# Kernel optimization log

Hardware: AMD Instinct MI355X
Metric: run time of the kernel (lower is better)

Reference implementation:

```python
import jax, jax.numpy as jnp
import numpy as np

MARGIN = 0.1
PERM_SEED = 42  # fixed stand-in for torch.randperm per row


def setup_inputs() -> dict:
    key = jax.random.key(0)
    k1, k2, k3 = jax.random.split(key, 3)
    n, d, f = 32768, 1000, 300
    inputs = jax.random.normal(k1, (n, f), dtype=jnp.float32)
    Y = jax.random.normal(k2, (d, f), dtype=jnp.float32)
    y_idxs = jax.random.randint(k3, (n,), 0, d)
    return {"inputs": inputs, "Y": Y, "y_idxs": y_idxs}


def reference(inputs, Y, y_idxs):
    # inputs: [n, f], Y: [d, f] class semantic embeddings, y_idxs: [n]
    n, d = inputs.shape[0], Y.shape[0]

    # All dot products at once: S[i, j] = Y[j] . inputs[i]
    S = inputs @ Y.T  # [n, d]

    # One random class permutation per row (torch.randperm(d) per sample)
    perm_keys = jax.random.split(jax.random.key(PERM_SEED), n)
    perms = jax.vmap(lambda k: jax.random.permutation(k, d))(perm_keys)  # [n, d]

    ap = S[jnp.arange(n), y_idxs]                 # [n]   anchor-positive dots
    an = jnp.take_along_axis(S, perms, axis=1)    # [n, d] anchor-negative dots in perm order

    valid = perms != y_idxs[:, None]              # skip j == y
    # early-break condition at each permutation slot
    cond = valid & ((ap[:, None] - an) > MARGIN)
    c = cond.astype(jnp.int32)
    excl_cum = jnp.cumsum(c, axis=1) - c          # exclusive cumsum of break events
    # include every valid slot up to AND including the first breaking slot
    include = valid & (excl_cum == 0)             # [n, d]

    # MarginRankingLoss with target=1: mean(max(0, margin + an - ap))
    per_pair = jnp.maximum(0.0, MARGIN + an - ap[:, None])
    total = jnp.sum(jnp.where(include, per_pair, 0.0))
    count = jnp.maximum(jnp.sum(include), 1).astype(jnp.float32)
    return total / count
```

## Files before the change

kernel.cpp:

```cpp
#include <hip/hip_runtime.h>
#include <stdint.h>

#define N_ROWS 32768
#define D_CLS  1000
#define D_PAD  1024
#define F_DIM  300
#define F_PAD  320
#define MARGIN 0.1f

#define BM     128
#define BN     128
#define BK     64
#define GTHR   512
#define KGTHR  1024
#define LDTA   328
#define LDTB   72

#define M_PB   32
#define NTHR   512
#define NT_PW  8
#define MT_PB  2
#define LDA    328
#define SROW   34

#define NPART  32

typedef short short8 __attribute__((ext_vector_type(8)));
typedef float f32x4  __attribute__((ext_vector_type(4)));

__device__ __forceinline__ uint32_t rotl32(uint32_t x, int r) {
  return (x << r) | (x >> (32 - r));
}

__device__ __forceinline__ void threefry2x32(uint32_t k0, uint32_t k1,
                                             uint32_t x0, uint32_t x1,
                                             uint32_t& o0, uint32_t& o1) {
  uint32_t k2 = k0 ^ k1 ^ 0x1BD11BDAu;
  x0 += k0; x1 += k1;
#define TF_R(r) { x0 += x1; x1 = rotl32(x1, (r)); x1 ^= x0; }
  TF_R(13) TF_R(15) TF_R(26) TF_R(6)
  x0 += k1; x1 += k2 + 1u;
  TF_R(17) TF_R(29) TF_R(16) TF_R(24)
  x0 += k2; x1 += k0 + 2u;
  TF_R(13) TF_R(15) TF_R(26) TF_R(6)
  x0 += k0; x1 += k1 + 3u;
  TF_R(17) TF_R(29) TF_R(16) TF_R(24)
  x0 += k1; x1 += k2 + 4u;
  TF_R(13) TF_R(15) TF_R(26) TF_R(6)
  x0 += k2; x1 += k0 + 5u;
#undef TF_R
  o0 = x0; o1 = x1;
}

struct TFSched {
  uint32_t k0, k1, k2, k2p1, k0p2, k1p3, k2p4, k0p5;
};
__device__ __forceinline__ TFSched tf_make(uint32_t k0, uint32_t k1) {
  TFSched s;
  s.k0 = k0; s.k1 = k1;
  s.k2 = k0 ^ k1 ^ 0x1BD11BDAu;
  s.k2p1 = s.k2 + 1u; s.k0p2 = k0 + 2u; s.k1p3 = k1 + 3u;
  s.k2p4 = s.k2 + 4u; s.k0p5 = k0 + 5u;
  return s;
}
__device__ __forceinline__ uint32_t tf_hash(const TFSched& s, uint32_t c) {
  uint32_t x0 = s.k0, x1 = c + s.k1;
#define TFH(r) { x0 += x1; x1 = __builtin_amdgcn_alignbit(x1, x1, 32 - (r)); x1 ^= x0; }
  TFH(13) TFH(15) TFH(26) TFH(6)
  x0 += s.k1; x1 += s.k2p1;
  TFH(17) TFH(29) TFH(16) TFH(24)
  x0 += s.k2; x1 += s.k0p2;
  TFH(13) TFH(15) TFH(26) TFH(6)
  x0 += s.k0; x1 += s.k1p3;
  TFH(17) TFH(29) TFH(16) TFH(24)
  x0 += s.k1; x1 += s.k2p4;
  TFH(13) TFH(15) TFH(26) TFH(6)
  x0 += s.k2; x1 += s.k0p5;
#undef TFH
  return x0 ^ x1;
}

__device__ __forceinline__ uint16_t f2bf(float f) {
  uint32_t u = __builtin_bit_cast(uint32_t, f);
  return (uint16_t)((u + 0x7FFFu + ((u >> 16) & 1u)) >> 16);
}
__device__ __forceinline__ float bf2f(uint16_t v) {
  return __builtin_bit_cast(float, (uint32_t)v << 16);
}
__device__ __forceinline__ float bf2f_lo(uint32_t v) {
  return __builtin_bit_cast(float, v << 16);
}
__device__ __forceinline__ float bf2f_hi(uint32_t v) {
  return __builtin_bit_cast(float, v & 0xFFFF0000u);
}

__device__ __forceinline__ void keygen_rp(uint32_t* __restrict__ keyP,
                                          const uint32_t* __restrict__ subk,
                                          int r0, int rp_loc, int lane) {
  const size_t rpg = (size_t)(r0 >> 1) + rp_loc;
  const int rA = r0 + 2 * rp_loc;
  const uint4 sk4 = *(const uint4*)(subk + 2 * rA);
  const TFSched sA = tf_make(sk4.x, sk4.y);
  const TFSched sB = tf_make(sk4.z, sk4.w);
#pragma unroll
  for (int chunk = 0; chunk < 4; ++chunk) {
    const uint32_t c0 = (uint32_t)(chunk * 256 + 4 * lane);
    uint32_t o[4];
#pragma unroll
    for (int j = 0; j < 4; ++j) {
      uint32_t kA = tf_hash(sA, c0 + (uint32_t)j);
      uint32_t kB = tf_hash(sB, c0 + (uint32_t)j);
      o[j] = (kA >> 16) | (kB & 0xFFFF0000u);
    }
    uint4 ov; ov.x = o[0]; ov.y = o[1]; ov.z = o[2]; ov.w = o[3];
    *(uint4*)(keyP + (rpg << 10) + c0) = ov;
  }
}

__global__ void prep(const float* __restrict__ Y, uint16_t* __restrict__ Ybf,
                     uint32_t* __restrict__ subk) {
  int i = blockIdx.x * 256 + threadIdx.x;
  if (i < D_PAD * F_PAD) {
    int j = i / F_PAD;
    int k = i - j * F_PAD;
    float v = (j < D_CLS && k < F_DIM) ? Y[j * F_DIM + k] : 0.f;
    Ybf[i] = f2bf(v);
  }
  if (i < N_ROWS) {
    uint32_t r1, r2, s1, s2;
    threefry2x32(0u, 42u, 0u, (uint32_t)i, r1, r2);
    threefry2x32(r1, r2, 0u, 1u, s1, s2);
    subk[2 * i]     = s1;
    subk[2 * i + 1] = s2;
  }
}

__launch_bounds__(KGTHR, 4)
__global__ void gk2(const float* __restrict__ inputs,
                    const uint16_t* __restrict__ Ybf,
                    uint32_t* __restrict__ Spair,
                    uint32_t* __restrict__ keyP,
                    const uint32_t* __restrict__ subk) {
  __shared__ __align__(16) uint16_t A_lds[BM * LDTA];

  const int t    = threadIdx.x;
  const int wave = t >> 6;
  const int lane = t & 63;
  const int l15  = lane & 15;
  const int g    = lane >> 4;
  const int r0   = blockIdx.x * BM;

  for (int i = t; i < BM * (F_DIM / 4); i += KGTHR) {
    int r  = i / 75;
    int c4 = i - r * 75;
    float4 v = *(const float4*)(inputs + (size_t)(r0 + r) * F_DIM + c4 * 4);
    ushort4 o;
    o.x = f2bf(v.x); o.y = f2bf(v.y); o.z = f2bf(v.z); o.w = f2bf(v.w);
    *(ushort4*)&A_lds[r * LDTA + c4 * 4] = o;
  }
  for (int i = t; i < BM * 7; i += KGTHR) {
    int r = i / 7, p = i - r * 7;
    *(ushort4*)&A_lds[r * LDTA + 300 + p * 4] = (ushort4){0, 0, 0, 0};
  }
  __syncthreads();

  if (wave < 8) {
    const int wm = wave >> 1;
    const int wn = wave & 1;
    const uint16_t* aBase = &A_lds[(wm * 32 + l15) * LDTA + g * 8];

#pragma unroll 1
    for (int cn = 0; cn < 8; ++cn) {
      f32x4 acc[2][4];
#pragma unroll
      for (int mt = 0; mt < 2; ++mt)
#pragma unroll
        for (int nt = 0; nt < 4; ++nt) acc[mt][nt] = (f32x4){0.f, 0.f, 0.f, 0.f};

      const uint16_t* gB[4];
#pragma unroll
      for (int nt = 0; nt < 4; ++nt) {
        const int col = cn * 128 + wn * 64 + nt * 16 + l15;
        gB[nt] = Ybf + (size_t)col * F_PAD + g * 8;
      }

#pragma unroll 2
      for (int ks = 0; ks < F_PAD / 32; ++ks) {
        short8 a[2], b[4];
#pragma unroll
        for (int nt = 0; nt < 4; ++nt)
          b[nt] = *(const short8*)(gB[nt] + ks * 32);
#pragma unroll
        for (int mt = 0; mt < 2; ++mt)
          a[mt] = *(const short8*)(aBase + mt * 16 * LDTA + ks * 32);
#pragma unroll
        for (int mt = 0; mt < 2; ++mt)
#pragma unroll
          for (int nt = 0; nt < 4; ++nt)
            acc[mt][nt] = __builtin_amdgcn_mfma_f32_16x16x32_bf16(a[mt], b[nt], acc[mt][nt], 0, 0, 0);
      }

#pragma unroll
      for (int mt = 0; mt < 2; ++mt)
#pragma unroll
        for (int nt = 0; nt < 4; ++nt) {
          const int col = cn * 128 + wn * 64 + nt * 16 + l15;
#pragma unroll
          for (int p = 0; p < 2; ++p) {
            uint32_t lo = f2bf(acc[mt][nt][2 * p]);
            uint32_t hi = f2bf(acc[mt][nt][2 * p + 1]);
            size_t rp = (size_t)(r0 >> 1) + wm * 16 + mt * 8 + g * 2 + p;
            Spair[rp * D_PAD + col] = (hi << 16) | lo;
          }
        }
    }
#pragma unroll 1
    for (int i = 0; i < 2; ++i)
      keygen_rp(keyP, subk, r0, 48 + wave * 2 + i, lane);
  } else {
    const int kw = wave - 8;
#pragma unroll 1
    for (int i = 0; i < 6; ++i)
      keygen_rp(keyP, subk, r0, kw * 6 + i, lane);
  }
}

__launch_bounds__(256, 4)
__global__ void loss_light(const uint32_t* __restrict__ Spair,
                           const uint32_t* __restrict__ keyP,
                           const int* __restrict__ yidx,
                           float* __restrict__ rowSum,
                           int* __restrict__ rowCnt) {
  const int lane = threadIdx.x & 63;
  const int wave = threadIdx.x >> 6;
  const int rp   = blockIdx.x * 4 + wave;
  const int rA   = 2 * rp;
  const int rB   = rA + 1;
  const int yA = yidx[rA], yB = yidx[rB];
  const uint32_t* Sp = Spair + (size_t)rp * D_PAD;
  const uint32_t* Kp = keyP  + (size_t)rp * D_PAD;
  const float apA = bf2f_lo(Sp[yA]);
  const float apB = bf2f_hi(Sp[yB]);

  uint32_t an[16], kk[16];
#pragma unroll
  for (int q4 = 0; q4 < 4; ++q4) {
    uint4 v = *(const uint4*)(Sp + q4 * 256 + lane * 4);
    an[4 * q4 + 0] = v.x; an[4 * q4 + 1] = v.y;
    an[4 * q4 + 2] = v.z; an[4 * q4 + 3] = v.w;
    uint4 w = *(const uint4*)(Kp + q4 * 256 + lane * 4);
    kk[4 * q4 + 0] = w.x; kk[4 * q4 + 1] = w.y;
    kk[4 * q4 + 2] = w.z; kk[4 * q4 + 3] = w.w;
  }

  uint32_t mnA = 0xFFFFu, mnB = 0xFFFFu;
#pragma unroll
  for (int q = 0; q < 16; ++q) {
    const int c = (q >> 2) * 256 + lane * 4 + (q & 3);
    const uint32_t kA = kk[q] & 0xFFFFu, kB = kk[q] >> 16;
    const float anA = bf2f_lo(an[q]), anB = bf2f_hi(an[q]);
    if ((c < D_CLS) && (c != yA) && (apA - anA) > MARGIN) mnA = (kA < mnA) ? kA : mnA;
    if ((c < D_CLS) && (c != yB) && (apB - anB) > MARGIN) mnB = (kB < mnB) ? kB : mnB;
  }
#pragma unroll
  for (int off = 1; off < 64; off <<= 1) {
    uint32_t oA = __shfl_xor(mnA, off, 64);
    uint32_t oB = __shfl_xor(mnB, off, 64);
    mnA = (oA < mnA) ? oA : mnA;
    mnB = (oB < mnB) ? oB : mnB;
  }

  float smA = 0.f, smB = 0.f; int ctA = 0, ctB = 0;
#pragma unroll
  for (int q = 0; q < 16; ++q) {
    const int c = (q >> 2) * 256 + lane * 4 + (q & 3);
    const uint32_t kA = kk[q] & 0xFFFFu, kB = kk[q] >> 16;
    const float anA = bf2f_lo(an[q]), anB = bf2f_hi(an[q]);
    if ((c < D_CLS) && (c != yA) && kA < mnA) { smA += MARGIN + anA - apA; ctA += 1; }
    if ((c < D_CLS) && (c != yB) && kB < mnB) { smB += MARGIN + anB - apB; ctB += 1; }
  }
#pragma unroll
  for (int off = 1; off < 64; off <<= 1) {
    smA += __shfl_xor(smA, off, 64);
    smB += __shfl_xor(smB, off, 64);
    ctA += __shfl_xor(ctA, off, 64);
    ctB += __shfl_xor(ctB, off, 64);
  }
  if (lane == 0) {
    rowSum[rA] = smA;  rowCnt[rA] = ctA + (mnA != 0xFFFFu ? 1 : 0);
    rowSum[rB] = smB;  rowCnt[rB] = ctB + (mnB != 0xFFFFu ? 1 : 0);
  }
}

__launch_bounds__(GTHR, 1)
__global__ void gemm_s(const float* __restrict__ inputs,
                       const uint16_t* __restrict__ Ybf,
                       uint32_t* __restrict__ Spair) {
  __shared__ __align__(16) uint16_t A_lds[BM * LDTA];
  __shared__ __align__(16) uint16_t B_lds[2][BN * LDTB];

  const int t    = threadIdx.x;
  const int wave = t >> 6;
  const int lane = t & 63;
  const int l15  = lane & 15;
  const int g    = lane >> 4;
  const int wm   = wave >> 1;
  const int wn   = wave & 1;
  const int r0   = blockIdx.x * BM;

  for (int i = t; i < BM * (F_DIM / 4); i += GTHR) {
    int r  = i / 75;
    int c4 = i - r * 75;
    float4 v = *(const float4*)(inputs + (size_t)(r0 + r) * F_DIM + c4 * 4);
    ushort4 o;
    o.x = f2bf(v.x); o.y = f2bf(v.y); o.z = f2bf(v.z); o.w = f2bf(v.w);
    *(ushort4*)&A_lds[r * LDTA + c4 * 4] = o;
  }
  for (int i = t; i < BM * 7; i += GTHR) {
    int r = i / 7, p = i - r * 7;
    *(ushort4*)&A_lds[r * LDTA + 300 + p * 4] = (ushort4){0, 0, 0, 0};
  }

  const int brow = t >> 3, bkof = t & 7;
  short8 bv[2];
  auto LOADB = [&](int tile) {
    const int c0 = (tile / 5) * BN;
    const int k0 = (tile % 5) * BK;
#pragma unroll
    for (int j = 0; j < 2; ++j)
      bv[j] = *(const short8*)(Ybf + (size_t)(c0 + j * 64 + brow) * F_PAD + k0 + bkof * 8);
  };
  auto WRITEB = [&](int buf) {
#pragma unroll
    for (int j = 0; j < 2; ++j)
      *(short8*)&B_lds[buf][(j * 64 + brow) * LDTB + bkof * 8] = bv[j];
  };

  f32x4 acc[2][4];
#pragma unroll
  for (int mt = 0; mt < 2; ++mt)
#pragma unroll
    for (int nt = 0; nt < 4; ++nt) acc[mt][nt] = (f32x4){0.f, 0.f, 0.f, 0.f};

  LOADB(0);
  __syncthreads();
  WRITEB(0);
  __syncthreads();

  const int NT = 8 * 5;
#pragma unroll 1
  for (int tile = 0; tile < NT; ++tile) {
    const int kt = tile % 5;
    if (tile < NT - 1) LOADB(tile + 1);
    const uint16_t* Bc = B_lds[tile & 1];
#pragma unroll
    for (int ks = 0; ks < 2; ++ks) {
      short8 a[2], b[4];
#pragma unroll
      for (int mt = 0; mt < 2; ++mt)
        a[mt] = *(const short8*)&A_lds[(wm * 32 + mt * 16 + l15) * LDTA + kt * BK + ks * 32 + g * 8];
#pragma unroll
      for (int nt = 0; nt < 4; ++nt)
        b[nt] = *(const short8*)&Bc[(wn * 64 + nt * 16 + l15) * LDTB + ks * 32 + g * 8];
#pragma unroll
      for (int mt = 0; mt < 2; ++mt)
#pragma unroll
        for (int nt = 0; nt < 4; ++nt)
          acc[mt][nt] = __builtin_amdgcn_mfma_f32_16x16x32_bf16(a[mt], b[nt], acc[mt][nt], 0, 0, 0);
    }
    if (kt == 4) {
      const int c0 = (tile / 5) * BN;
#pragma unroll
      for (int mt = 0; mt < 2; ++mt)
#pragma unroll
        for (int nt = 0; nt < 4; ++nt) {
          const int col = c0 + wn * 64 + nt * 16 + l15;
#pragma unroll
          for (int p = 0; p < 2; ++p) {
            uint32_t lo = f2bf(acc[mt][nt][2 * p]);
            uint32_t hi = f2bf(acc[mt][nt][2 * p + 1]);
            size_t rp = (size_t)(r0 >> 1) + wm * 16 + mt * 8 + g * 2 + p;
            Spair[rp * D_PAD + col] = (hi << 16) | lo;
          }
          acc[mt][nt] = (f32x4){0.f, 0.f, 0.f, 0.f};
        }
    }
    if (tile < NT - 1) {
      WRITEB((tile + 1) & 1);
      __syncthreads();
    }
  }
}

__launch_bounds__(256, 2)
__global__ void hash_loss(const uint32_t* __restrict__ Spair,
                          const uint32_t* __restrict__ subk,
                          const int* __restrict__ yidx,
                          float* __restrict__ rowSum,
                          int* __restrict__ rowCnt) {
  const int lane = threadIdx.x & 63;
  const int wave = threadIdx.x >> 6;
  const int rp   = blockIdx.x * 4 + wave;
  const int rA   = 2 * rp;
  const int rB   = 2 * rp + 1;

  const int yA = yidx[rA], yB = yidx[rB];
  const TFSched sA = tf_make(subk[2 * rA], subk[2 * rA + 1]);
  const TFSched sB = tf_make(subk[2 * rB], subk[2 * rB + 1]);

  const uint32_t* Sp = Spair + (size_t)rp * D_PAD;
  const float apA = bf2f_lo(Sp[yA]);
  const float apB = bf2f_hi(Sp[yB]);

  uint32_t an[16];
#pragma unroll
  for (int j = 0; j < 4; ++j) {
    uint4 v = *(const uint4*)(Sp + j * 256 + lane * 4);
    an[4 * j + 0] = v.x; an[4 * j + 1] = v.y;
    an[4 * j + 2] = v.z; an[4 * j + 3] = v.w;
  }

  uint32_t skAB[16];
  uint32_t pkA = 0xFFFFFFFFu, pkB = 0xFFFFFFFFu;
#pragma unroll
  for (int q = 0; q < 16; ++q) {
    const int c = (q >> 2) * 256 + lane * 4 + (q & 3);
    uint32_t kA = tf_hash(sA, (uint32_t)c);
    uint32_t kB = tf_hash(sB, (uint32_t)c);
    skAB[q] = (kA >> 16) | (kB & 0xFFFF0000u);
    float anA = bf2f_lo(an[q]);
    float anB = bf2f_hi(an[q]);
    if ((c < D_CLS) && (c != yA) && (apA - anA) > MARGIN) {
      pkA = (kA < pkA) ? kA : pkA;
    }
    if ((c < D_CLS) && (c != yB) && (apB - anB) > MARGIN) {
      pkB = (kB < pkB) ? kB : pkB;
    }
  }
#pragma unroll
  for (int off = 1; off < 64; off <<= 1) {
    uint32_t oA = __shfl_xor(pkA, off, 64);
    uint32_t oB = __shfl_xor(pkB, off, 64);
    pkA = (oA < pkA) ? oA : pkA;
    pkB = (oB < pkB) ? oB : pkB;
  }
  const uint32_t pA16 = pkA >> 16;
  const uint32_t pB16 = pkB >> 16;

  float smA = 0.f, smB = 0.f; int ctA = 0, ctB = 0;
#pragma unroll
  for (int q = 0; q < 16; ++q) {
    const int c = (q >> 2) * 256 + lane * 4 + (q & 3);
    float anA = bf2f_lo(an[q]);
    float anB = bf2f_hi(an[q]);
    if ((c < D_CLS) && (c != yA) && (skAB[q] & 0xFFFFu) < pA16) {
      smA += MARGIN + anA - apA; ctA += 1;
    }
    if ((c < D_CLS) && (c != yB) && (skAB[q] >> 16) < pB16) {
      smB += MARGIN + anB - apB; ctB += 1;
    }
  }
#pragma unroll
  for (int off = 1; off < 64; off <<= 1) {
    smA += __shfl_xor(smA, off, 64);
    smB += __shfl_xor(smB, off, 64);
    ctA += __shfl_xor(ctA, off, 64);
    ctB += __shfl_xor(ctB, off, 64);
  }
  if (lane == 0) {
    rowSum[rA] = smA;
    rowCnt[rA] = ctA + (pkA != 0xFFFFFFFFu ? 1 : 0);
    rowSum[rB] = smB;
    rowCnt[rB] = ctB + (pkB != 0xFFFFFFFFu ? 1 : 0);
  }
}

__launch_bounds__(NTHR, 4)
__global__ void triplet_fused(const float* __restrict__ inputs,
                              const uint16_t* __restrict__ Ybf,
                              const int* __restrict__ yidx,
                              float* __restrict__ rowSum,
                              int* __restrict__ rowCnt) {
  __shared__ __align__(16) uint16_t SH[D_PAD * SROW];
  __shared__ int      y_sh[M_PB];
  __shared__ uint32_t subk_sh[M_PB][2];

  const int t    = threadIdx.x;
  const int wave = t >> 6;
  const int lane = t & 63;
  const int l15  = lane & 15;
  const int g    = lane >> 4;
  const int row0 = blockIdx.x * M_PB;
  const int colbase = wave * (NT_PW * 16);

  if (t < M_PB) {
    y_sh[t] = yidx[row0 + t];
    uint32_t r1, r2, s1, s2;
    threefry2x32(0u, 42u, 0u, (uint32_t)(row0 + t), r1, r2);
    threefry2x32(r1, r2, 0u, 1u, s1, s2);
    subk_sh[t][0] = s1; subk_sh[t][1] = s2;
  }

  uint16_t* A_fl = SH;
  for (int i = t; i < M_PB * (F_DIM / 4); i += NTHR) {
    int r  = i / 75;
    int c4 = i - r * 75;
    float4 v = *(const float4*)(inputs + (size_t)(row0 + r) * F_DIM + c4 * 4);
    ushort4 o;
    o.x = f2bf(v.x); o.y = f2bf(v.y); o.z = f2bf(v.z); o.w = f2bf(v.w);
    *(ushort4*)&A_fl[r * LDA + c4 * 4] = o;
  }
  for (int i = t; i < M_PB * 5; i += NTHR) {
    int r = i / 5, p = i - r * 5;
    *(ushort4*)&A_fl[r * LDA + 300 + p * 4] = (ushort4){0, 0, 0, 0};
  }
  __syncthreads();

  f32x4 acc[MT_PB][NT_PW];
#pragma unroll
  for (int mt = 0; mt < MT_PB; ++mt)
#pragma unroll
    for (int nt = 0; nt < NT_PW; ++nt) acc[mt][nt] = (f32x4){0.f, 0.f, 0.f, 0.f};

  const uint16_t* gB[NT_PW];
#pragma unroll
  for (int nt = 0; nt < NT_PW; ++nt) {
    int j = colbase + nt * 16 + l15;
    gB[nt] = Ybf + (size_t)j * F_PAD + (g << 3);
  }
  const uint16_t* aBase = &A_fl[l15 * LDA + (g << 3)];

#pragma unroll 2
  for (int ks = 0; ks < F_PAD / 32; ++ks) {
    short8 b[NT_PW], a[MT_PB];
#pragma unroll
    for (int nt = 0; nt < NT_PW; ++nt)
      b[nt] = *(const short8*)(gB[nt] + ks * 32);
#pragma unroll
    for (int mt = 0; mt < MT_PB; ++mt)
      a[mt] = *(const short8*)(aBase + mt * 16 * LDA + ks * 32);
#pragma unroll
    for (int mt = 0; mt < MT_PB; ++mt)
#pragma unroll
      for (int nt = 0; nt < NT_PW; ++nt)
        acc[mt][nt] = __builtin_amdgcn_mfma_f32_16x16x32_bf16(a[mt], b[nt], acc[mt][nt], 0, 0, 0);
  }

  __syncthreads();

#pragma unroll
  for (int mt = 0; mt < MT_PB; ++mt)
#pragma unroll
    for (int nt = 0; nt < NT_PW; ++nt) {
      int col = colbase + nt * 16 + l15;
#pragma unroll
      for (int p = 0; p < 2; ++p) {
        uint32_t lo = f2bf(acc[mt][nt][2 * p]);
        uint32_t hi = f2bf(acc[mt][nt][2 * p + 1]);
        *(uint32_t*)&SH[col * SROW + mt * 16 + (g << 2) + 2 * p] = (hi << 16) | lo;
      }
    }
  __syncthreads();

#pragma unroll
  for (int pr = 0; pr < 2; ++pr) {
    const int rA = wave * 4 + pr * 2;
    const int rB = rA + 1;
    const int yA = y_sh[rA], yB = y_sh[rB];
    const uint32_t a1 = subk_sh[rA][0], a2 = subk_sh[rA][1];
    const uint32_t b1 = subk_sh[rB][0], b2 = subk_sh[rB][1];
    const float apA = bf2f(SH[yA * SROW + rA]);
    const float apB = bf2f(SH[yB * SROW + rB]);

    uint32_t skA[16], skB[16];
    uint32_t pkA = 0xFFFFFFFFu, pkB = 0xFFFFFFFFu;
#pragma unroll
    for (int q = 0; q < 16; ++q) {
      const int c = q * 64 + lane;
      uint32_t xA, yAo, xB, yBo;
      threefry2x32(a1, a2, 0u, (uint32_t)c, xA, yAo);
      threefry2x32(b1, b2, 0u, (uint32_t)c, xB, yBo);
      skA[q] = xA ^ yAo;
      skB[q] = xB ^ yBo;
      float anA = bf2f(SH[c * SROW + rA]);
      float anB = bf2f(SH[c * SROW + rB]);
      if ((c < D_CLS) && (c != yA) && (apA - anA) > MARGIN) {
        pkA = (skA[q] < pkA) ? skA[q] : pkA;
      }
      if ((c < D_CLS) && (c != yB) && (apB - anB) > MARGIN) {
        pkB = (skB[q] < pkB) ? skB[q] : pkB;
      }
    }
#pragma unroll
    for (int off = 1; off < 64; off <<= 1) {
      uint32_t oA = __shfl_xor(pkA, off, 64);
      uint32_t oB = __shfl_xor(pkB, off, 64);
      pkA = (oA < pkA) ? oA : pkA;
      pkB = (oB < pkB) ? oB : pkB;
    }
    float smA = 0.f, smB = 0.f; int ctA = 0, ctB = 0;
#pragma unroll
    for (int q = 0; q < 16; ++q) {
      const int c = q * 64 + lane;
      float anA = bf2f(SH[c * SROW + rA]);
      float anB = bf2f(SH[c * SROW + rB]);
      if ((c < D_CLS) && (c != yA) && skA[q] < pkA) { smA += MARGIN + anA - apA; ctA += 1; }
      if ((c < D_CLS) && (c != yB) && skB[q] < pkB) { smB += MARGIN + anB - apB; ctB += 1; }
    }
#pragma unroll
    for (int off = 1; off < 64; off <<= 1) {
      smA += __shfl_xor(smA, off, 64);
      smB += __shfl_xor(smB, off, 64);
      ctA += __shfl_xor(ctA, off, 64);
      ctB += __shfl_xor(ctB, off, 64);
    }
    if (lane == 0) {
      rowSum[row0 + rA] = smA;
      rowCnt[row0 + rA] = ctA + (pkA != 0xFFFFFFFFu ? 1 : 0);
      rowSum[row0 + rB] = smB;
      rowCnt[row0 + rB] = ctB + (pkB != 0xFFFFFFFFu ? 1 : 0);
    }
  }
}

__global__ void reduce_part(const float* __restrict__ rowSum,
                            const int* __restrict__ rowCnt,
                            float* __restrict__ pS, int* __restrict__ pC) {
  __shared__ float ss[4];
  __shared__ int   sc[4];
  const int base = blockIdx.x * (N_ROWS / NPART);
  float s = 0.f; int c = 0;
  for (int i = threadIdx.x; i < N_ROWS / NPART; i += 256) {
    s += rowSum[base + i];
    c += rowCnt[base + i];
  }
#pragma unroll
  for (int off = 32; off > 0; off >>= 1) {
    s += __shfl_down(s, (unsigned)off, 64);
    c += __shfl_down(c, (unsigned)off, 64);
  }
  int wid = threadIdx.x >> 6, lane = threadIdx.x & 63;
  if (lane == 0) { ss[wid] = s; sc[wid] = c; }
  __syncthreads();
  if (threadIdx.x == 0) {
    pS[blockIdx.x] = ss[0] + ss[1] + ss[2] + ss[3];
    pC[blockIdx.x] = sc[0] + sc[1] + sc[2] + sc[3];
  }
}

__global__ void reduce_final(const float* __restrict__ pS,
                             const int* __restrict__ pC,
                             float* __restrict__ out) {
  const int lane = threadIdx.x;
  float s = (lane < NPART) ? pS[lane] : 0.f;
  int   c = (lane < NPART) ? pC[lane] : 0;
#pragma unroll
  for (int off = 32; off > 0; off >>= 1) {
    s += __shfl_down(s, (unsigned)off, 64);
    c += __shfl_down(c, (unsigned)off, 64);
  }
  if (lane == 0) out[0] = s / (float)(c < 1 ? 1 : c);
}

extern "C" void kernel_launch(void* const* d_in, const int* in_sizes, int n_in,
                              void* d_out, int out_size, void* d_ws, size_t ws_size,
                              hipStream_t stream) {
  const float* inputs = (const float*)d_in[0];
  const float* Y      = (const float*)d_in[1];
  const int*   yidx   = (const int*)d_in[2];
  float* out = (float*)d_out;

  char* ws = (char*)d_ws;
  size_t off = 0;
  uint16_t* Ybf    = (uint16_t*)(ws + off); off += (size_t)D_PAD * F_PAD * 2;
  float*    rowSum = (float*)(ws + off);    off += (size_t)N_ROWS * 4;
  int*      rowCnt = (int*)(ws + off);      off += (size_t)N_ROWS * 4;
  uint32_t* subk   = (uint32_t*)(ws + off); off += (size_t)N_ROWS * 8;
  float*    pS     = (float*)(ws + off);    off += (size_t)NPART * 4;
  int*      pC     = (int*)(ws + off);      off += (size_t)NPART * 4;
  off = (off + 255) & ~(size_t)255;
  uint32_t* Spair  = (uint32_t*)(ws + off); off += (size_t)(N_ROWS / 2) * D_PAD * 4;
  const size_t need_mid = off;
  off = (off + 255) & ~(size_t)255;
  uint32_t* keyP   = (uint32_t*)(ws + off); off += (size_t)(N_ROWS / 2) * D_PAD * 4;
  const size_t need_full = off;

  hipLaunchKernelGGL(prep, dim3((D_PAD * F_PAD + 255) / 256), dim3(256),
                     0, stream, Y, Ybf, subk);
  if (ws_size >= need_full) {
    hipLaunchKernelGGL(gk2, dim3(N_ROWS / BM), dim3(KGTHR),
                       0, stream, inputs, Ybf, Spair, keyP, subk);
    hipLaunchKernelGGL(loss_light, dim3(N_ROWS / 8), dim3(256),
                       0, stream, Spair, keyP, yidx, rowSum, rowCnt);
  } else if (ws_size >= need_mid) {
    hipLaunchKernelGGL(gemm_s, dim3(N_ROWS / BM), dim3(GTHR),
                       0, stream, inputs, Ybf, Spair);
    hipLaunchKernelGGL(hash_loss, dim3(N_ROWS / 8), dim3(256),
                       0, stream, Spair, subk, yidx, rowSum, rowCnt);
  } else {
    hipLaunchKernelGGL(triplet_fused, dim3(N_ROWS / M_PB), dim3(NTHR),
                       0, stream, inputs, Ybf, yidx, rowSum, rowCnt);
  }
  hipLaunchKernelGGL(reduce_part, dim3(NPART), dim3(256), 0, stream,
                     rowSum, rowCnt, pS, pC);
  hipLaunchKernelGGL(reduce_final, dim3(1), dim3(64), 0, stream, pS, pC, out);
}
```

Measured before the change: 133.0 us.

## Split GEMM and permutation-key generation into separate interleaved blocks

Replaces the 1024-thread block, in which some waves ran the GEMM and others generated threefry permutation keys, with 512-thread blocks that each take one role. Role is chosen by a blockIdx bit, so GEMM and keygen blocks alternate in groups of eight. GEMM blocks now cover 64 rows with 8 waves each holding a 2x2 MFMA tile, and keygen blocks each handle 32 row pairs. The aim is better occupancy and overlap of compute-bound hashing with MFMA work across CUs. In exchange there are more blocks, each GEMM block loads B for fewer rows (more redundant Y reads), and LDS per block is smaller.

Result: slower. 187.9 us (+41.3%).

```diff
diff --git a/kernel.cpp b/kernel.cpp
--- a/kernel.cpp
+++ b/kernel.cpp
@@ -8,12 +8,17 @@
 #define F_PAD  320
 #define MARGIN 0.1f
 
+#define GBM    64
+#define GKTHR  512
+#define LDTA   328
+#define NGB    (N_ROWS / GBM)
+#define RP_PB  32
+#define NKB    ((N_ROWS / 2) / RP_PB)
+
 #define BM     128
 #define BN     128
 #define BK     64
 #define GTHR   512
-#define KGTHR  1024
-#define LDTA   328
 #define LDTB   72
 
 #define M_PB   32
@@ -94,11 +99,10 @@
   return __builtin_bit_cast(float, v & 0xFFFF0000u);
 }
 
-__device__ __forceinline__ void keygen_rp(uint32_t* __restrict__ keyP,
-                                          const uint32_t* __restrict__ subk,
-                                          int r0, int rp_loc, int lane) {
-  const size_t rpg = (size_t)(r0 >> 1) + rp_loc;
-  const int rA = r0 + 2 * rp_loc;
+__device__ __forceinline__ void keygen_rp_g(uint32_t* __restrict__ keyP,
+                                            const uint32_t* __restrict__ subk,
+                                            size_t rpg, int lane) {
+  const int rA = 2 * (int)rpg;
   const uint4 sk4 = *(const uint4*)(subk + 2 * rA);
   const TFSched sA = tf_make(sk4.x, sk4.y);
   const TFSched sB = tf_make(sk4.z, sk4.w);
@@ -135,76 +139,74 @@
   }
 }
 
-__launch_bounds__(KGTHR, 4)
-__global__ void gk2(const float* __restrict__ inputs,
+__launch_bounds__(GKTHR, 6)
+__global__ void gkb(const float* __restrict__ inputs,
                     const uint16_t* __restrict__ Ybf,
                     uint32_t* __restrict__ Spair,
                     uint32_t* __restrict__ keyP,
                     const uint32_t* __restrict__ subk) {
-  __shared__ __align__(16) uint16_t A_lds[BM * LDTA];
+  __shared__ __align__(16) uint16_t A_lds[GBM * LDTA];
 
   const int t    = threadIdx.x;
   const int wave = t >> 6;
   const int lane = t & 63;
   const int l15  = lane & 15;
   const int g    = lane >> 4;
-  const int r0   = blockIdx.x * BM;
-
-  for (int i = t; i < BM * (F_DIM / 4); i += KGTHR) {
-    int r  = i / 75;
-    int c4 = i - r * 75;
-    float4 v = *(const float4*)(inputs + (size_t)(r0 + r) * F_DIM + c4 * 4);
-    ushort4 o;
-    o.x = f2bf(v.x); o.y = f2bf(v.y); o.z = f2bf(v.z); o.w = f2bf(v.w);
-    *(ushort4*)&A_lds[r * LDTA + c4 * 4] = o;
-  }
-  for (int i = t; i < BM * 7; i += KGTHR) {
-    int r = i / 7, p = i - r * 7;
-    *(ushort4*)&A_lds[r * LDTA + 300 + p * 4] = (ushort4){0, 0, 0, 0};
-  }
-  __syncthreads();
-
-  if (wave < 8) {
-    const int wm = wave >> 1;
-    const int wn = wave & 1;
+  const int role = (blockIdx.x >> 3) & 1;
+  const int sub  = (blockIdx.x >> 4) * 8 + (blockIdx.x & 7);
+
+  if (role == 0) {
+    const int r0 = sub * GBM;
+
+    for (int i = t; i < GBM * (F_DIM / 4); i += GKTHR) {
+      int r  = i / 75;
+      int c4 = i - r * 75;
+      float4 v = *(const float4*)(inputs + (size_t)(r0 + r) * F_DIM + c4 * 4);
+      ushort4 o;
+      o.x = f2bf(v.x); o.y = f2bf(v.y); o.z = f2bf(v.z); o.w = f2bf(v.w);
+      *(ushort4*)&A_lds[r * LDTA + c4 * 4] = o;
+    }
+    for (int i = t; i < GBM * 7; i += GKTHR) {
+      int r = i / 7, p = i - r * 7;
+      *(ushort4*)&A_lds[r * LDTA + 300 + p * 4] = (ushort4){0, 0, 0, 0};
+    }
+    __syncthreads();
+
+    const int wm = wave >> 2;
+    const int wn = wave & 3;
     const uint16_t* aBase = &A_lds[(wm * 32 + l15) * LDTA + g * 8];
 
 #pragma unroll 1
     for (int cn = 0; cn < 8; ++cn) {
-      f32x4 acc[2][4];
+      f32x4 acc[2][2];
 #pragma unroll
       for (int mt = 0; mt < 2; ++mt)
 #pragma unroll
-        for (int nt = 0; nt < 4; ++nt) acc[mt][nt] = (f32x4){0.f, 0.f, 0.f, 0.f};
-
-      const uint16_t* gB[4];
-#pragma unroll
-      for (int nt = 0; nt < 4; ++nt) {
-        const int col = cn * 128 + wn * 64 + nt * 16 + l15;
-        gB[nt] = Ybf + (size_t)col * F_PAD + g * 8;
-      }
+        for (int nt = 0; nt < 2; ++nt) acc[mt][nt] = (f32x4){0.f, 0.f, 0.f, 0.f};
+
+      const uint16_t* gBp = Ybf + (size_t)(cn * 128 + wn * 32 + l15) * F_PAD + g * 8;
 
 #pragma unroll 2
       for (int ks = 0; ks < F_PAD / 32; ++ks) {
-        short8 a[2], b[4];
-#pragma unroll
-        for (int nt = 0; nt < 4; ++nt)
-          b[nt] = *(const short8*)(gB[nt] + ks * 32);
+        short8 a[2], b[2];
+#pragma unroll
+        for (int nt = 0; nt < 2; ++nt)
+          b[nt] = *(const short8*)(gBp + (size_t)nt * 16 * F_PAD + ks * 32);
 #pragma unroll
         for (int mt = 0; mt < 2; ++mt)
           a[mt] = *(const short8*)(aBase + mt * 16 * LDTA + ks * 32);
 #pragma unroll
         for (int mt = 0; mt < 2; ++mt)
 #pragma unroll
-          for (int nt = 0; nt < 4; ++nt)
+          for (int nt = 0; nt < 2; ++nt)
             acc[mt][nt] = __builtin_amdgcn_mfma_f32_16x16x32_bf16(a[mt], b[nt], acc[mt][nt], 0, 0, 0);
       }
 
 #pragma unroll
       for (int mt = 0; mt < 2; ++mt)
 #pragma unroll
-        for (int nt = 0; nt < 4; ++nt) {
-          const int col = cn * 128 + wn * 64 + nt * 16 + l15;
+        for (int nt = 0; nt < 2; ++nt) {
+          const int col = cn * 128 + wn * 32 + nt * 16 + l15;
 #pragma unroll
           for (int p = 0; p < 2; ++p) {
             uint32_t lo = f2bf(acc[mt][nt][2 * p]);
@@ -214,14 +216,11 @@
           }
         }
     }
+  } else {
+    const size_t rp0 = (size_t)sub * RP_PB + (size_t)wave * 4;
 #pragma unroll 1
-    for (int i = 0; i < 2; ++i)
-      keygen_rp(keyP, subk, r0, 48 + wave * 2 + i, lane);
-  } else {
-    const int kw = wave - 8;
-#pragma unroll 1
-    for (int i = 0; i < 6; ++i)
-      keygen_rp(keyP, subk, r0, kw * 6 + i, lane);
+    for (int i = 0; i < 4; ++i)
+      keygen_rp_g(keyP, subk, rp0 + i, lane);
   }
 }
 
@@ -688,7 +687,7 @@
   hipLaunchKernelGGL(prep, dim3((D_PAD * F_PAD + 255) / 256), dim3(256),
                      0, stream, Y, Ybf, subk);
   if (ws_size >= need_full) {
-    hipLaunchKernelGGL(gk2, dim3(N_ROWS / BM), dim3(KGTHR),
+    hipLaunchKernelGGL(gkb, dim3(NGB + NKB), dim3(GKTHR),
                        0, stream, inputs, Ybf, Spair, keyP, subk);
     hipLaunchKernelGGL(loss_light, dim3(N_ROWS / 8), dim3(256),
                        0, stream, Spair, keyP, yidx, rowSum, rowCnt);
```

## Fuse loss pass into GEMM/keygen kernel with 64-row blocks

Applied to the files above, without the earlier changes.

Merges the separate loss_light kernel into the GEMM+keygen kernel. Each block now handles 64 rows with a 2x4 wave layout over 256-column chunks, and after a block barrier every wave computes the loss for two row-pairs, reading Spair and keyP that were just written (likely still in L2). This removes one kernel launch and the global round trip between the kernels, and halves the LDS tile so more blocks can be resident. In exchange the loss loop reloads Spair/keyP twice instead of holding them in registers, and each Ybf column now feeds only 64 rows, which raises B-operand traffic.

Result: slower. 142.1 us (+6.9%).

```diff
diff --git a/kernel.cpp b/kernel.cpp
--- a/kernel.cpp
+++ b/kernel.cpp
@@ -8,12 +8,14 @@
 #define F_PAD  320
 #define MARGIN 0.1f
 
+#define G3BM   64
+#define G3THR  1024
+#define LDTA   328
+
 #define BM     128
 #define BN     128
 #define BK     64
 #define GTHR   512
-#define KGTHR  1024
-#define LDTA   328
 #define LDTB   72
 
 #define M_PB   32
@@ -135,22 +137,25 @@
   }
 }
 
-__launch_bounds__(KGTHR, 4)
-__global__ void gk2(const float* __restrict__ inputs,
+__launch_bounds__(G3THR, 8)
+__global__ void gk3(const float* __restrict__ inputs,
                     const uint16_t* __restrict__ Ybf,
                     uint32_t* __restrict__ Spair,
                     uint32_t* __restrict__ keyP,
-                    const uint32_t* __restrict__ subk) {
-  __shared__ __align__(16) uint16_t A_lds[BM * LDTA];
+                    const uint32_t* __restrict__ subk,
+                    const int* __restrict__ yidx,
+                    float* __restrict__ rowSum,
+                    int* __restrict__ rowCnt) {
+  __shared__ __align__(16) uint16_t A_lds[G3BM * LDTA];
 
   const int t    = threadIdx.x;
   const int wave = t >> 6;
   const int lane = t & 63;
   const int l15  = lane & 15;
   const int g    = lane >> 4;
-  const int r0   = blockIdx.x * BM;
-
-  for (int i = t; i < BM * (F_DIM / 4); i += KGTHR) {
+  const int r0   = blockIdx.x * G3BM;
+
+  for (int i = t; i < G3BM * (F_DIM / 4); i += G3THR) {
     int r  = i / 75;
     int c4 = i - r * 75;
     float4 v = *(const float4*)(inputs + (size_t)(r0 + r) * F_DIM + c4 * 4);
@@ -158,19 +163,19 @@
     o.x = f2bf(v.x); o.y = f2bf(v.y); o.z = f2bf(v.z); o.w = f2bf(v.w);
     *(ushort4*)&A_lds[r * LDTA + c4 * 4] = o;
   }
-  for (int i = t; i < BM * 7; i += KGTHR) {
+  for (int i = t; i < G3BM * 7; i += G3THR) {
     int r = i / 7, p = i - r * 7;
     *(ushort4*)&A_lds[r * LDTA + 300 + p * 4] = (ushort4){0, 0, 0, 0};
   }
   __syncthreads();
 
   if (wave < 8) {
-    const int wm = wave >> 1;
-    const int wn = wave & 1;
+    const int wm = wave >> 2;
+    const int wn = wave & 3;
     const uint16_t* aBase = &A_lds[(wm * 32 + l15) * LDTA + g * 8];
 
 #pragma unroll 1
-    for (int cn = 0; cn < 8; ++cn) {
+    for (int cn = 0; cn < 4; ++cn) {
       f32x4 acc[2][4];
 #pragma unroll
       for (int mt = 0; mt < 2; ++mt)
@@ -180,7 +185,7 @@
       const uint16_t* gB[4];
 #pragma unroll
       for (int nt = 0; nt < 4; ++nt) {
-        const int col = cn * 128 + wn * 64 + nt * 16 + l15;
+        const int col = cn * 256 + wn * 64 + nt * 16 + l15;
         gB[nt] = Ybf + (size_t)col * F_PAD + g * 8;
       }
 
@@ -204,7 +209,7 @@
       for (int mt = 0; mt < 2; ++mt)
 #pragma unroll
         for (int nt = 0; nt < 4; ++nt) {
-          const int col = cn * 128 + wn * 64 + nt * 16 + l15;
+          const int col = cn * 256 + wn * 64 + nt * 16 + l15;
 #pragma unroll
           for (int p = 0; p < 2; ++p) {
             uint32_t lo = f2bf(acc[mt][nt][2 * p]);
@@ -214,81 +219,78 @@
           }
         }
     }
-#pragma unroll 1
-    for (int i = 0; i < 2; ++i)
-      keygen_rp(keyP, subk, r0, 48 + wave * 2 + i, lane);
+    keygen_rp(keyP, subk, r0, 24 + wave, lane);
   } else {
     const int kw = wave - 8;
 #pragma unroll 1
-    for (int i = 0; i < 6; ++i)
-      keygen_rp(keyP, subk, r0, kw * 6 + i, lane);
-  }
-}
-
-__launch_bounds__(256, 4)
-__global__ void loss_light(const uint32_t* __restrict__ Spair,
-                           const uint32_t* __restrict__ keyP,
-                           const int* __restrict__ yidx,
-                           float* __restrict__ rowSum,
-                           int* __restrict__ rowCnt) {
-  const int lane = threadIdx.x & 63;
-  const int wave = threadIdx.x >> 6;
-  const int rp   = blockIdx.x * 4 + wave;
-  const int rA   = 2 * rp;
-  const int rB   = rA + 1;
-  const int yA = yidx[rA], yB = yidx[rB];
-  const uint32_t* Sp = Spair + (size_t)rp * D_PAD;
-  const uint32_t* Kp = keyP  + (size_t)rp * D_PAD;
-  const float apA = bf2f_lo(Sp[yA]);
-  const float apB = bf2f_hi(Sp[yB]);
-
-  uint32_t an[16], kk[16];
-#pragma unroll
-  for (int q4 = 0; q4 < 4; ++q4) {
-    uint4 v = *(const uint4*)(Sp + q4 * 256 + lane * 4);
-    an[4 * q4 + 0] = v.x; an[4 * q4 + 1] = v.y;
-    an[4 * q4 + 2] = v.z; an[4 * q4 + 3] = v.w;
-    uint4 w = *(const uint4*)(Kp + q4 * 256 + lane * 4);
-    kk[4 * q4 + 0] = w.x; kk[4 * q4 + 1] = w.y;
-    kk[4 * q4 + 2] = w.z; kk[4 * q4 + 3] = w.w;
-  }
-
-  uint32_t mnA = 0xFFFFu, mnB = 0xFFFFu;
-#pragma unroll
-  for (int q = 0; q < 16; ++q) {
-    const int c = (q >> 2) * 256 + lane * 4 + (q & 3);
-    const uint32_t kA = kk[q] & 0xFFFFu, kB = kk[q] >> 16;
-    const float anA = bf2f_lo(an[q]), anB = bf2f_hi(an[q]);
-    if ((c < D_CLS) && (c != yA) && (apA - anA) > MARGIN) mnA = (kA < mnA) ? kA : mnA;
-    if ((c < D_CLS) && (c != yB) && (apB - anB) > MARGIN) mnB = (kB < mnB) ? kB : mnB;
-  }
-#pragma unroll
-  for (int off = 1; off < 64; off <<= 1) {
-    uint32_t oA = __shfl_xor(mnA, off, 64);
-    uint32_t oB = __shfl_xor(mnB, off, 64);
-    mnA = (oA < mnA) ? oA : mnA;
-    mnB = (oB < mnB) ? oB : mnB;
-  }
-
-  float smA = 0.f, smB = 0.f; int ctA = 0, ctB = 0;
-#pragma unroll
-  for (int q = 0; q < 16; ++q) {
-    const int c = (q >> 2) * 256 + lane * 4 + (q & 3);
-    const uint32_t kA = kk[q] & 0xFFFFu, kB = kk[q] >> 16;
-    const float anA = bf2f_lo(an[q]), anB = bf2f_hi(an[q]);
-    if ((c < D_CLS) && (c != yA) && kA < mnA) { smA += MARGIN + anA - apA; ctA += 1; }
-    if ((c < D_CLS) && (c != yB) && kB < mnB) { smB += MARGIN + anB - apB; ctB += 1; }
-  }
-#pragma unroll
-  for (int off = 1; off < 64; off <<= 1) {
-    smA += __shfl_xor(smA, off, 64);
-    smB += __shfl_xor(smB, off, 64);
-    ctA += __shfl_xor(ctA, off, 64);
-    ctB += __shfl_xor(ctB, off, 64);
-  }
-  if (lane == 0) {
-    rowSum[rA] = smA;  rowCnt[rA] = ctA + (mnA != 0xFFFFu ? 1 : 0);
-    rowSum[rB] = smB;  rowCnt[rB] = ctB + (mnB != 0xFFFFu ? 1 : 0);
+    for (int i = 0; i < 3; ++i)
+      keygen_rp(keyP, subk, r0, kw * 3 + i, lane);
+  }
+
+  __syncthreads();
+
+#pragma unroll 1
+  for (int j = 0; j < 2; ++j) {
+    const int rp_loc = wave * 2 + j;
+    const size_t rpg = (size_t)(r0 >> 1) + rp_loc;
+    const int rA = r0 + 2 * rp_loc;
+    const int yA = yidx[rA], yB = yidx[rA + 1];
+    const uint32_t* Sp = Spair + (rpg << 10);
+    const uint32_t* Kp = keyP  + (rpg << 10);
+    const float apA = bf2f_lo(Sp[yA]);
+    const float apB = bf2f_hi(Sp[yB]);
+
+    uint32_t mnA = 0xFFFFu, mnB = 0xFFFFu;
+#pragma unroll 1
+    for (int q4 = 0; q4 < 4; ++q4) {
+      uint4 v = *(const uint4*)(Sp + q4 * 256 + lane * 4);
+      uint4 w = *(const uint4*)(Kp + q4 * 256 + lane * 4);
+      uint32_t an4[4] = {v.x, v.y, v.z, v.w};
+      uint32_t kk4[4] = {w.x, w.y, w.z, w.w};
+#pragma unroll
+      for (int jj = 0; jj < 4; ++jj) {
+        const int c = q4 * 256 + lane * 4 + jj;
+        const uint32_t kA = kk4[jj] & 0xFFFFu, kB = kk4[jj] >> 16;
+        const float anA = bf2f_lo(an4[jj]), anB = bf2f_hi(an4[jj]);
+        if ((c < D_CLS) && (c != yA) && (apA - anA) > MARGIN) mnA = (kA < mnA) ? kA : mnA;
+        if ((c < D_CLS) && (c != yB) && (apB - anB) > MARGIN) mnB = (kB < mnB) ? kB : mnB;
+      }
+    }
+#pragma unroll
+    for (int off = 1; off < 64; off <<= 1) {
+      uint32_t oA = __shfl_xor(mnA, off, 64);
+      uint32_t oB = __shfl_xor(mnB, off, 64);
+      mnA = (oA < mnA) ? oA : mnA;
+      mnB = (oB < mnB) ? oB : mnB;
+    }
+
+    float smA = 0.f, smB = 0.f; int ctA = 0, ctB = 0;
+#pragma unroll 1
+    for (int q4 = 0; q4 < 4; ++q4) {
+      uint4 v = *(const uint4*)(Sp + q4 * 256 + lane * 4);
+      uint4 w = *(const uint4*)(Kp + q4 * 256 + lane * 4);
+      uint32_t an4[4] = {v.x, v.y, v.z, v.w};
+      uint32_t kk4[4] = {w.x, w.y, w.z, w.w};
+#pragma unroll
+      for (int jj = 0; jj < 4; ++jj) {
+        const int c = q4 * 256 + lane * 4 + jj;
+        const uint32_t kA = kk4[jj] & 0xFFFFu, kB = kk4[jj] >> 16;
+        const float anA = bf2f_lo(an4[jj]), anB = bf2f_hi(an4[jj]);
+        if ((c < D_CLS) && (c != yA) && kA < mnA) { smA += MARGIN + anA - apA; ctA += 1; }
+        if ((c < D_CLS) && (c != yB) && kB < mnB) { smB += MARGIN + anB - apB; ctB += 1; }
+      }
+    }
+#pragma unroll
+    for (int off = 1; off < 64; off <<= 1) {
+      smA += __shfl_xor(smA, off, 64);
+      smB += __shfl_xor(smB, off, 64);
+      ctA += __shfl_xor(ctA, off, 64);
+      ctB += __shfl_xor(ctB, off, 64);
+    }
+    if (lane == 0) {
+      rowSum[rA]     = smA;  rowCnt[rA]     = ctA + (mnA != 0xFFFFu ? 1 : 0);
+      rowSum[rA + 1] = smB;  rowCnt[rA + 1] = ctB + (mnB != 0xFFFFu ? 1 : 0);
+    }
   }
 }
 
@@ -688,10 +690,9 @@
   hipLaunchKernelGGL(prep, dim3((D_PAD * F_PAD + 255) / 256), dim3(256),
                      0, stream, Y, Ybf, subk);
   if (ws_size >= need_full) {
-    hipLaunchKernelGGL(gk2, dim3(N_ROWS / BM), dim3(KGTHR),
-                       0, stream, inputs, Ybf, Spair, keyP, subk);
-    hipLaunchKernelGGL(loss_light, dim3(N_ROWS / 8), dim3(256),
-                       0, stream, Spair, keyP, yidx, rowSum, rowCnt);
+    hipLaunchKernelGGL(gk3, dim3(N_ROWS / G3BM), dim3(G3THR),
+                       0, stream, inputs, Ybf, Spair, keyP, subk,
+                       yidx, rowSum, rowCnt);
   } else if (ws_size >= need_mid) {
     hipLaunchKernelGGL(gemm_s, dim3(N_ROWS / BM), dim3(GTHR),
                        0, stream, inputs, Ybf, Spair);
```
